# Kernel optimization log

Hardware: AMD Instinct MI355X
Metric: run time of the kernel (lower is better)

## Reference

```python
import jax, jax.numpy as jnp
import numpy as np
import math

NUM_BUCKETS = 32
MAX_DISTANCE = 128
N_HEADS = 16
D_KV = 64
D_MODEL = 1024


def _relative_position_bucket(relative_position, num_buckets=NUM_BUCKETS, max_distance=MAX_DISTANCE):
    # bidirectional (encoder) variant
    num_buckets = num_buckets // 2
    relative_buckets = (relative_position > 0).astype(jnp.int32) * num_buckets
    relative_position = jnp.abs(relative_position)
    max_exact = num_buckets // 2
    is_small = relative_position < max_exact
    # avoid log(0); masked by is_small anyway
    rp = jnp.maximum(relative_position, 1).astype(jnp.float32)
    rel_if_large = max_exact + (
        jnp.log(rp / max_exact) / math.log(max_distance / max_exact) * (num_buckets - max_exact)
    ).astype(jnp.int32)
    rel_if_large = jnp.minimum(rel_if_large, num_buckets - 1)
    relative_buckets = relative_buckets + jnp.where(is_small, relative_position, rel_if_large)
    return relative_buckets


def compute_bias(rel_bias, q_len, k_len):
    context = jnp.arange(q_len, dtype=jnp.int32)[:, None]
    memory = jnp.arange(k_len, dtype=jnp.int32)[None, :]
    buckets = _relative_position_bucket(memory - context)  # [q,k]
    values = rel_bias[buckets]                              # [q,k,H]
    return jnp.transpose(values, (2, 0, 1))[None]           # [1,H,q,k]


def setup_inputs() -> dict:
    key = jax.random.key(0)
    k1, k2, k3, k4 = jax.random.split(key, 4)
    B, S = 2, 2048
    hidden_states = jax.random.normal(k1, (B, S, D_MODEL), dtype=jnp.float32)
    attention_mask = jnp.ones((B, S), dtype=jnp.int32)
    w_qkv = jax.random.normal(k2, (3 * D_MODEL, D_MODEL), dtype=jnp.float32) * 0.02
    rel_bias = jax.random.normal(k3, (NUM_BUCKETS, N_HEADS), dtype=jnp.float32)
    w_o = jax.random.normal(k4, (D_MODEL, D_MODEL), dtype=jnp.float32) * 0.02
    return {"hidden_states": hidden_states, "attention_mask": attention_mask,
            "w_qkv": w_qkv, "rel_bias": rel_bias, "w_o": w_o}


def reference(hidden_states, attention_mask, w_qkv, rel_bias, w_o):
    B, S, _ = hidden_states.shape
    n, c = N_HEADS, D_KV
    qkv = hidden_states @ w_qkv.T                      # [B,S,3*inner]
    q, k, v = jnp.split(qkv, 3, axis=-1)
    q = q.reshape(B, S, n, c)
    k = k.reshape(B, S, n, c)
    v = v.reshape(B, S, n, c)
    attn_bias = jnp.broadcast_to(compute_bias(rel_bias, S, S), (B, n, S, S))
    mask = attention_mask.reshape(B, 1, 1, S)
    mask_val = jnp.finfo(q.dtype).min
    attn_bias = jnp.where(mask == 0, mask_val, attn_bias)
    attn = jnp.einsum('binc,bjnc->bnij', q, k) + attn_bias   # no 1/sqrt(d) scale in T5
    attn = jax.nn.softmax(attn.astype(jnp.float32), axis=-1).astype(q.dtype)
    x = jnp.einsum('bnij,bjnc->binc', attn, v)
    x = x.reshape(B, S, n * c)
    return x @ w_o.T
```

## Files before the change

kernel.cpp:

```cpp
#include <hip/hip_runtime.h>
#include <stdint.h>

typedef __attribute__((ext_vector_type(4))) float f32x4;
typedef __attribute__((ext_vector_type(8))) short short8;
typedef __attribute__((ext_vector_type(4))) short short4v;
typedef __attribute__((ext_vector_type(2))) unsigned uint2v;

__device__ __forceinline__ short f2bf(float f) {
    union { float f; unsigned u; } x; x.f = f;
    return (short)((x.u + 0x7fffu + ((x.u >> 16) & 1u)) >> 16);
}

__device__ __forceinline__ unsigned cvt_pk_bf16(float lo, float hi) {
    unsigned r;
    asm("v_cvt_pk_bf16_f32 %0, %1, %2" : "=v"(r) : "v"(lo), "v"(hi));
    return r;
}

__device__ __forceinline__ float fexp2(float x) {
#if __has_builtin(__builtin_amdgcn_exp2f)
    return __builtin_amdgcn_exp2f(x);
#else
    return exp2f(x);
#endif
}

#define MFMA16(a, b, c) __builtin_amdgcn_mfma_f32_16x16x32_bf16((a), (b), (c), 0, 0, 0)

__device__ __forceinline__ void gload16(const void* g, void* l) {
    __builtin_amdgcn_global_load_lds((const __attribute__((address_space(1))) void*)g,
                                     (__attribute__((address_space(3))) void*)l, 16, 0, 0);
}

__global__ __launch_bounds__(256) void cast_all(const float* __restrict__ h,
                                                const float* __restrict__ wq,
                                                const float* __restrict__ wo,
                                                short* __restrict__ hb,
                                                short* __restrict__ wqb,
                                                short* __restrict__ wob) {
    int i = blockIdx.x * 256 + threadIdx.x;
    const float* s;
    short* d;
    int j;
    if (i < 524288) { s = h; d = hb; j = i; }
    else if (i < 917504) { s = wq; d = wqb; j = i - 524288; }
    else { s = wo; d = wob; j = i - 917504; }
    float4 a = ((const float4*)s)[j * 2];
    float4 b = ((const float4*)s)[j * 2 + 1];
    short8 o;
    o[0] = f2bf(a.x); o[1] = f2bf(a.y); o[2] = f2bf(a.z); o[3] = f2bf(a.w);
    o[4] = f2bf(b.x); o[5] = f2bf(b.y); o[6] = f2bf(b.z); o[7] = f2bf(b.w);
    ((short8*)d)[j] = o;
}

template <int OUT_BF16, int QSCALE>
__global__ __launch_bounds__(512, 2) void gemm8p(const short* __restrict__ A,
                                                 const short* __restrict__ B,
                                                 void* __restrict__ Cout,
                                                 int M, int N, int K) {
    __shared__ short lds[2][4][8192];
    const int t = threadIdx.x;
    const int l = t & 63, w = t >> 6;
    const int lr = l & 15, lg = l >> 4;
    const int wr = w >> 2, wc = w & 3;
    const int m0 = blockIdx.y * 256, n0 = blockIdx.x * 256;
    const int nt = K >> 6, nh = nt << 2;

    const int sr0 = t >> 2;
    const int scc = ((t & 3) ^ ((sr0 >> 1) & 3)) * 8;
    const short* As0 = A + (size_t)(m0 + sr0) * K + scc;
    const short* As1 = A + (size_t)(m0 + sr0 + 128) * K + scc;
    const short* Bs0 = B + (size_t)(n0 + sr0) * K + scc;
    const short* Bs1 = B + (size_t)(n0 + sr0 + 128) * K + scc;
    short* ldsb = &lds[0][0][0];

    auto stageH = [&](int H) {
        int Tp = H >> 2, pos = H & 3;
        int kb = Tp * 64 + ((pos <= 1) ? 32 : 0);
        short* dst = ldsb + ((Tp & 1) * 4 + pos) * 8192 + t * 8;
        if (pos & 1) {
            gload16(As0 + kb, dst);
            gload16(As1 + kb, dst + 4096);
        } else {
            gload16(Bs0 + kb, dst);
            gload16(Bs1 + kb, dst + 4096);
        }
    };

    int aoff[8], boff[4];
    #pragma unroll
    for (int mi = 0; mi < 8; ++mi) {
        int row = wr * 128 + mi * 16 + lr;
        aoff[mi] = row * 32 + (lg ^ ((row >> 1) & 3)) * 8;
    }
    #pragma unroll
    for (int ni = 0; ni < 4; ++ni) {
        int row = wc * 64 + ni * 16 + lr;
        boff[ni] = row * 32 + (lg ^ ((row >> 1) & 3)) * 8;
    }

    f32x4 acc[8][4] = {};

    for (int H = 0; H < 7; ++H) stageH(H);
    asm volatile("s_waitcnt vmcnt(6)" ::: "memory");
    __builtin_amdgcn_s_barrier();

    for (int T = 0; T < nt; ++T) {
        const short* rbase = ldsb + (T & 1) * 32768;
        const short* B1b = rbase;
        const short* A1b = rbase + 8192;
        const short* B0b = rbase + 16384;
        const short* A0b = rbase + 24576;
        const int Hs = (T << 2) + 7;
        short8 a[4], b[4];

        #pragma unroll
        for (int i = 0; i < 4; ++i) a[i] = *(const short8*)(A1b + aoff[i]);
        #pragma unroll
        for (int i = 0; i < 4; ++i) b[i] = *(const short8*)(B1b + boff[i]);
        if (Hs < nh) stageH(Hs);
        __builtin_amdgcn_sched_barrier(0);
        __builtin_amdgcn_s_barrier();
        asm volatile("s_waitcnt lgkmcnt(0)" ::: "memory");
        __builtin_amdgcn_sched_barrier(0);
        __builtin_amdgcn_s_setprio(1);
        #pragma unroll
        for (int mi = 0; mi < 4; ++mi)
            #pragma unroll
            for (int ni = 0; ni < 4; ++ni)
                acc[mi][ni] = MFMA16(a[mi], b[ni], acc[mi][ni]);
        __builtin_amdgcn_s_setprio(0);
        __builtin_amdgcn_sched_barrier(0);
        __builtin_amdgcn_s_barrier();

        #pragma unroll
        for (int i = 0; i < 4; ++i) a[i] = *(const short8*)(A1b + aoff[4 + i]);
        if (Hs + 1 < nh) stageH(Hs + 1);
        __builtin_amdgcn_sched_barrier(0);
        __builtin_amdgcn_s_barrier();
        asm volatile("s_waitcnt lgkmcnt(0)" ::: "memory");
        __builtin_amdgcn_sched_barrier(0);
        __builtin_amdgcn_s_setprio(1);
        #pragma unroll
        for (int mi = 0; mi < 4; ++mi)
            #pragma unroll
            for (int ni = 0; ni < 4; ++ni)
                acc[4 + mi][ni] = MFMA16(a[mi], b[ni], acc[4 + mi][ni]);
        __builtin_amdgcn_s_setprio(0);
        __builtin_amdgcn_sched_barrier(0);
        __builtin_amdgcn_s_barrier();

        #pragma unroll
        for (int i = 0; i < 4; ++i) a[i] = *(const short8*)(A0b + aoff[i]);
        #pragma unroll
        for (int i = 0; i < 4; ++i) b[i] = *(const short8*)(B0b + boff[i]);
        if (Hs + 2 < nh) stageH(Hs + 2);
        __builtin_amdgcn_sched_barrier(0);
        __builtin_amdgcn_s_barrier();
        asm volatile("s_waitcnt lgkmcnt(0)" ::: "memory");
        __builtin_amdgcn_sched_barrier(0);
        __builtin_amdgcn_s_setprio(1);
        #pragma unroll
        for (int mi = 0; mi < 4; ++mi)
            #pragma unroll
            for (int ni = 0; ni < 4; ++ni)
                acc[mi][ni] = MFMA16(a[mi], b[ni], acc[mi][ni]);
        __builtin_amdgcn_s_setprio(0);
        __builtin_amdgcn_sched_barrier(0);
        __builtin_amdgcn_s_barrier();

        #pragma unroll
        for (int i = 0; i < 4; ++i) a[i] = *(const short8*)(A0b + aoff[4 + i]);
        if (Hs + 3 < nh) stageH(Hs + 3);
        __builtin_amdgcn_sched_barrier(0);
        __builtin_amdgcn_s_barrier();
        asm volatile("s_waitcnt lgkmcnt(0)" ::: "memory");
        __builtin_amdgcn_sched_barrier(0);
        __builtin_amdgcn_s_setprio(1);
        #pragma unroll
        for (int mi = 0; mi < 4; ++mi)
            #pragma unroll
            for (int ni = 0; ni < 4; ++ni)
                acc[4 + mi][ni] = MFMA16(a[mi], b[ni], acc[4 + mi][ni]);
        __builtin_amdgcn_s_setprio(0);
        if (T < nt - 2) {
            asm volatile("s_waitcnt vmcnt(6)" ::: "memory");
        } else if (T == nt - 2) {
            asm volatile("s_waitcnt vmcnt(0)" ::: "memory");
        }
        __builtin_amdgcn_sched_barrier(0);
        __builtin_amdgcn_s_barrier();
    }

    const float qs = (QSCALE && n0 < 1024) ? 1.4426950408889634f : 1.0f;
    #pragma unroll
    for (int mi = 0; mi < 8; ++mi)
        #pragma unroll
        for (int ni = 0; ni < 4; ++ni)
            #pragma unroll
            for (int rr = 0; rr < 4; ++rr) {
                int mm = m0 + wr * 128 + mi * 16 + lg * 4 + rr;
                int nn = n0 + wc * 64 + ni * 16 + lr;
                float v = acc[mi][ni][rr] * qs;
                if (OUT_BF16) ((short*)Cout)[(size_t)mm * N + nn] = f2bf(v);
                else ((float*)Cout)[(size_t)mm * N + nn] = v;
            }
}

template <int OUT_BF16, int QSCALE>
__global__ __launch_bounds__(256) void gemm_bt(const short* __restrict__ A,
                                               const short* __restrict__ B,
                                               void* __restrict__ Cout,
                                               int M, int N, int K) {
    __shared__ short sA[4096];
    __shared__ short sB[4096];
    const int t = threadIdx.x;
    const int l = t & 63, w = t >> 6;
    const int lr = l & 15, lg = l >> 4;
    const int m0 = blockIdx.y * 128, n0 = blockIdx.x * 128;
    const int wm = (w >> 1) * 64, wn = (w & 1) * 64;
    const int c0 = w * 64 + l, c1 = c0 + 256;
    const short* Ap0 = A + (size_t)(m0 + (c0 >> 2)) * K + (c0 & 3) * 8;
    const short* Ap1 = A + (size_t)(m0 + (c1 >> 2)) * K + (c1 & 3) * 8;
    const short* Bp0 = B + (size_t)(n0 + (c0 >> 2)) * K + (c0 & 3) * 8;
    const short* Bp1 = B + (size_t)(n0 + (c1 >> 2)) * K + (c1 & 3) * 8;
    short* lA0 = sA + w * 512;
    short* lA1 = sA + 2048 + w * 512;
    short* lB0 = sB + w * 512;
    short* lB1 = sB + 2048 + w * 512;
    f32x4 acc[4][4] = {};
    for (int k0 = 0; k0 < K; k0 += 32) {
        gload16(Ap0 + k0, lA0);
        gload16(Ap1 + k0, lA1);
        gload16(Bp0 + k0, lB0);
        gload16(Bp1 + k0, lB1);
        __syncthreads();
        short8 af[4], bfr[4];
        #pragma unroll
        for (int m = 0; m < 4; ++m) af[m] = *(const short8*)&sA[(wm + m * 16 + lr) * 32 + lg * 8];
        #pragma unroll
        for (int n = 0; n < 4; ++n) bfr[n] = *(const short8*)&sB[(wn + n * 16 + lr) * 32 + lg * 8];
        #pragma unroll
        for (int m = 0; m < 4; ++m)
            #pragma unroll
            for (int n = 0; n < 4; ++n)
                acc[m][n] = MFMA16(af[m], bfr[n], acc[m][n]);
        __syncthreads();
    }
    const float qs = (QSCALE && n0 < 1024) ? 1.4426950408889634f : 1.0f;
    #pragma unroll
    for (int m = 0; m < 4; ++m)
        #pragma unroll
        for (int n = 0; n < 4; ++n)
            #pragma unroll
            for (int r = 0; r < 4; ++r) {
                int mm = m0 + wm + m * 16 + lg * 4 + r;
                int nn = n0 + wn + n * 16 + lr;
                float v = acc[m][n][r] * qs;
                if (OUT_BF16) ((short*)Cout)[(size_t)mm * N + nn] = f2bf(v);
                else ((float*)Cout)[(size_t)mm * N + nn] = v;
            }
}

__global__ __launch_bounds__(256) void transpose_v(const short* __restrict__ qkv,
                                                   short* __restrict__ vt) {
    __shared__ short T[64][72];
    const int t = threadIdx.x;
    const int s0 = blockIdx.x * 64, bh = blockIdx.y;
    const int b = bh >> 4, h = bh & 15;
    const int rl = t >> 2, cg = (t & 3) * 16;
    const short* src = qkv + (size_t)(b * 2048 + s0 + rl) * 3072 + 2048 + h * 64 + cg;
    *(short8*)&T[rl][cg] = *(const short8*)src;
    *(short8*)&T[rl][cg + 8] = *(const short8*)(src + 8);
    __syncthreads();
    short8 o0, o1;
    #pragma unroll
    for (int e = 0; e < 8; ++e) o0[e] = T[cg + e][rl];
    #pragma unroll
    for (int e = 0; e < 8; ++e) o1[e] = T[cg + 8 + e][rl];
    short* dst = vt + ((size_t)bh * 64 + rl) * 2048 + s0 + cg;
    *(short8*)dst = o0;
    *(short8*)(dst + 8) = o1;
}

__global__ __launch_bounds__(512, 4) void attn_kernel(const short* __restrict__ qkv,
                                                      const short* __restrict__ vt,
                                                      const int* __restrict__ amask,
                                                      const float* __restrict__ rel_bias,
                                                      short* __restrict__ xout) {
    __shared__ float tbl[340];
    __shared__ short sK[4096];
    __shared__ short sV[4096];
    __shared__ short sP[8][16][72];
    __shared__ int mflags[32];
    const int t = threadIdx.x;
    const int l = t & 63, w = t >> 6;
    const int lr = l & 15, lg = l >> 4;
    const int qt = blockIdx.x, bh = blockIdx.y;
    const int b = bh >> 4, h = bh & 15;
    const int q0 = qt * 128 + w * 16;
    const float LOG2E = 1.4426950408889634f;

    if (t < 32) mflags[t] = ~0;
    if (t < 337) {
        int idx = t;
        int d = idx - 168;
        int a = d < 0 ? -d : d;
        int fb = a < 8 ? a
                 : (a < 12 ? 8 : a < 16 ? 9 : a < 23 ? 10 : a < 32 ? 11
                    : a < 46 ? 12 : a < 64 ? 13 : a < 91 ? 14 : 15);
        int bk = (d > 0 ? 16 : 0) + fb;
        tbl[idx] = rel_bias[bk * 16 + h] * LOG2E;
    }
    const float rbp = rel_bias[31 * 16 + h] * LOG2E;
    const float rbn = rel_bias[15 * 16 + h] * LOG2E;

    short8 qf[2];
    #pragma unroll
    for (int ds = 0; ds < 2; ++ds)
        qf[ds] = *(const short8*)(qkv + (size_t)(b * 2048 + q0 + lr) * 3072 + h * 64 + ds * 32 + lg * 8);

    const int4 ma = ((const int4*)(amask + b * 2048))[t];

    const int srow = t >> 3;
    const int scp = ((t & 7) ^ (srow & 7)) * 8;
    const short* kgp = qkv + (size_t)(b * 2048 + srow) * 3072 + 1024 + h * 64 + scp;
    const short* vgp = vt + ((size_t)bh * 64 + srow) * 2048 + scp;
    short* dK = sK + t * 8;
    short* dV = sV + t * 8;
    const int sw8 = (lr & 7) * 8;
    const int ibb = -q0 + lg * 4 - lr + 168;

    __syncthreads();
    int mok = ma.x & ma.y & ma.z & ma.w;
    if (mok == 0) atomicAnd(&mflags[t >> 4], 0);

    f32x4 o[4] = {};
    float mreg = -1e30f, lreg = 0.f;

    for (int kt = 0; kt < 2048; kt += 64) {
        gload16(kgp + (size_t)kt * 3072, dK);
        gload16(vgp + kt, dV);
        __syncthreads();

        f32x4 pe[4];
        #pragma unroll
        for (int ct = 0; ct < 4; ++ct) {
            f32x4 z = {};
            #pragma unroll
            for (int ds = 0; ds < 2; ++ds) {
                short8 kf = *(const short8*)&sK[(ct * 16 + lr) * 64 + ((ds * 32 + lg * 8) ^ sw8)];
                z = MFMA16(kf, qf[ds], z);
            }
            pe[ct] = z;
        }

        float cb;
        if (kt >= q0 + 106) {
            cb = rbp;
        } else if (kt + 63 <= q0 - 91) {
            cb = rbn;
        } else {
            cb = 0.f;
            const int ib = kt + ibb;
            #pragma unroll
            for (int ct = 0; ct < 4; ++ct)
                #pragma unroll
                for (int r = 0; r < 4; ++r)
                    pe[ct][r] += tbl[ib + ct * 16 + r];
        }

        float t0 = fmaxf(fmaxf(pe[0][0], pe[0][1]), fmaxf(pe[0][2], pe[0][3]));
        float t1 = fmaxf(fmaxf(pe[1][0], pe[1][1]), fmaxf(pe[1][2], pe[1][3]));
        float t2 = fmaxf(fmaxf(pe[2][0], pe[2][1]), fmaxf(pe[2][2], pe[2][3]));
        float t3 = fmaxf(fmaxf(pe[3][0], pe[3][1]), fmaxf(pe[3][2], pe[3][3]));
        float lmax = fmaxf(fmaxf(t0, t1), fmaxf(t2, t3));
        if (__any(lmax > mreg - cb + 11.5f)) {
            float rm = fmaxf(lmax, __shfl_xor(lmax, 16));
            rm = fmaxf(rm, __shfl_xor(rm, 32));
            float mnew = fmaxf(mreg, rm + cb);
            float alpha = fexp2(mreg - mnew);
            lreg *= alpha;
            #pragma unroll
            for (int dt = 0; dt < 4; ++dt)
                #pragma unroll
                for (int r = 0; r < 4; ++r)
                    o[dt][r] *= alpha;
            mreg = mnew;
        }
        const float madj = mreg - cb;
        const int tok = mflags[kt >> 6];
        float rs = 0.f;
        if (tok) {
            #pragma unroll
            for (int ct = 0; ct < 4; ++ct) {
                float p[4];
                #pragma unroll
                for (int r = 0; r < 4; ++r) {
                    float pv = fexp2(pe[ct][r] - madj);
                    p[r] = pv;
                    rs += pv;
                }
                uint2v pk;
                pk[0] = cvt_pk_bf16(p[0], p[1]);
                pk[1] = cvt_pk_bf16(p[2], p[3]);
                *(uint2v*)&sP[w][lr][ct * 16 + lg * 4] = pk;
            }
        } else {
            const int4* mp = (const int4*)(amask + b * 2048 + kt);
            #pragma unroll
            for (int ct = 0; ct < 4; ++ct) {
                int4 cm = mp[ct * 4 + lg];
                float p[4];
                #pragma unroll
                for (int r = 0; r < 4; ++r) {
                    float pv = fexp2(pe[ct][r] - madj);
                    pv = ((const int*)&cm)[r] ? pv : 0.f;
                    p[r] = pv;
                    rs += pv;
                }
                uint2v pk;
                pk[0] = cvt_pk_bf16(p[0], p[1]);
                pk[1] = cvt_pk_bf16(p[2], p[3]);
                *(uint2v*)&sP[w][lr][ct * 16 + lg * 4] = pk;
            }
        }
        lreg += rs;

        #pragma unroll
        for (int kk = 0; kk < 2; ++kk) {
            short8 pf = *(const short8*)&sP[w][lr][kk * 32 + lg * 8];
            #pragma unroll
            for (int dt = 0; dt < 4; ++dt) {
                short8 vf = *(const short8*)&sV[(dt * 16 + lr) * 64 + ((kk * 32 + lg * 8) ^ sw8)];
                o[dt] = MFMA16(vf, pf, o[dt]);
            }
        }
        __syncthreads();
    }

    float lsum = lreg + __shfl_xor(lreg, 16);
    lsum += __shfl_xor(lsum, 32);
    const float inv = 1.0f / lsum;
    #pragma unroll
    for (int dt = 0; dt < 4; ++dt) {
        short4v ov;
        #pragma unroll
        for (int r = 0; r < 4; ++r) ov[r] = f2bf(o[dt][r] * inv);
        *(short4v*)(xout + (size_t)(b * 2048 + q0 + lr) * 1024 + h * 64 + dt * 16 + lg * 4) = ov;
    }
}

extern "C" void kernel_launch(void* const* d_in, const int* in_sizes, int n_in,
                              void* d_out, int out_size, void* d_ws, size_t ws_size,
                              hipStream_t stream) {
    const float* hidden = (const float*)d_in[0];
    const int* amask = (const int*)d_in[1];
    const float* w_qkv = (const float*)d_in[2];
    const float* rel_bias = (const float*)d_in[3];
    const float* w_o = (const float*)d_in[4];
    if (ws_size < 58720256) return;
    char* ws = (char*)d_ws;
    short* hidden_bf = (short*)(ws + 0);
    short* wqkv_bf   = (short*)(ws + 8388608);
    short* wo_bf     = (short*)(ws + 14680064);
    short* qkv       = (short*)(ws + 16777216);
    short* vt        = (short*)(ws + 41943040);
    short* xbuf      = (short*)(ws + 50331648);

    cast_all<<<4096, 256, 0, stream>>>(hidden, w_qkv, w_o, hidden_bf, wqkv_bf, wo_bf);
    gemm8p<1, 1><<<dim3(12, 16), 512, 0, stream>>>(hidden_bf, wqkv_bf, qkv, 4096, 3072, 1024);
    transpose_v<<<dim3(32, 32), 256, 0, stream>>>(qkv, vt);
    attn_kernel<<<dim3(16, 32), 512, 0, stream>>>(qkv, vt, amask, rel_bias, xbuf);
    gemm_bt<0, 0><<<dim3(8, 32), 256, 0, stream>>>(xbuf, wo_bf, d_out, 4096, 1024, 1024);
}
```

Before: 135.1 us.

## Double-buffer K/V tiles in LDS to overlap global loads with compute

```diff
diff --git a/kernel.cpp b/kernel.cpp
--- a/kernel.cpp
+++ b/kernel.cpp
@@ -289,8 +289,8 @@
                                                       const float* __restrict__ rel_bias,
                                                       short* __restrict__ xout) {
     __shared__ float tbl[340];
-    __shared__ short sK[4096];
-    __shared__ short sV[4096];
+    __shared__ short sK[2][4096];
+    __shared__ short sV[2][4096];
     __shared__ short sP[8][16][72];
     __shared__ int mflags[32];
     const int t = threadIdx.x;
@@ -326,22 +326,35 @@
     const int scp = ((t & 7) ^ (srow & 7)) * 8;
     const short* kgp = qkv + (size_t)(b * 2048 + srow) * 3072 + 1024 + h * 64 + scp;
     const short* vgp = vt + ((size_t)bh * 64 + srow) * 2048 + scp;
-    short* dK = sK + t * 8;
-    short* dV = sV + t * 8;
     const int sw8 = (lr & 7) * 8;
     const int ibb = -q0 + lg * 4 - lr + 168;
 
     __syncthreads();
     int mok = ma.x & ma.y & ma.z & ma.w;
     if (mok == 0) atomicAnd(&mflags[t >> 4], 0);
+    __syncthreads();
+
+    gload16(kgp, &sK[0][0] + t * 8);
+    gload16(vgp, &sV[0][0] + t * 8);
 
     f32x4 o[4] = {};
     float mreg = -1e30f, lreg = 0.f;
 
     for (int kt = 0; kt < 2048; kt += 64) {
-        gload16(kgp + (size_t)kt * 3072, dK);
-        gload16(vgp + kt, dV);
-        __syncthreads();
+        const int cur = (kt >> 6) & 1;
+        if (kt + 64 < 2048) {
+            gload16(kgp + (size_t)(kt + 64) * 3072, &sK[cur ^ 1][0] + t * 8);
+            gload16(vgp + kt + 64, &sV[cur ^ 1][0] + t * 8);
+            asm volatile("s_waitcnt vmcnt(2)" ::: "memory");
+        } else {
+            asm volatile("s_waitcnt vmcnt(0)" ::: "memory");
+        }
+        __builtin_amdgcn_sched_barrier(0);
+        __builtin_amdgcn_s_barrier();
+        __builtin_amdgcn_sched_barrier(0);
+
+        const short* kb = &sK[cur][0];
+        const short* vb = &sV[cur][0];
 
         f32x4 pe[4];
         #pragma unroll
@@ -349,7 +362,7 @@
             f32x4 z = {};
             #pragma unroll
             for (int ds = 0; ds < 2; ++ds) {
-                short8 kf = *(const short8*)&sK[(ct * 16 + lr) * 64 + ((ds * 32 + lg * 8) ^ sw8)];
+                short8 kf = *(const short8*)&kb[(ct * 16 + lr) * 64 + ((ds * 32 + lg * 8) ^ sw8)];
                 z = MFMA16(kf, qf[ds], z);
             }
             pe[ct] = z;
@@ -432,11 +445,13 @@
             short8 pf = *(const short8*)&sP[w][lr][kk * 32 + lg * 8];
             #pragma unroll
             for (int dt = 0; dt < 4; ++dt) {
-                short8 vf = *(const short8*)&sV[(dt * 16 + lr) * 64 + ((kk * 32 + lg * 8) ^ sw8)];
+                short8 vf = *(const short8*)&vb[(dt * 16 + lr) * 64 + ((kk * 32 + lg * 8) ^ sw8)];
                 o[dt] = MFMA16(vf, pf, o[dt]);
             }
         }
-        __syncthreads();
+        __builtin_amdgcn_sched_barrier(0);
+        __builtin_amdgcn_s_barrier();
+        __builtin_amdgcn_sched_barrier(0);
     }
 
     float lsum = lreg + __shfl_xor(lreg, 16);
```

After: 134.7 us. Within noise of the previous version (-0.3%).
